# Kernel tuning notes

Measured on AMD Instinct MI355X. Metric: run time of the kernel, lower is better.

The kernel has to match this reference:

```python
import jax, jax.numpy as jnp
import numpy as np

OUT_FEATURES = 4096
IN_FEATURES = 4096
SCALE_EPS = 1e-5


def setup_inputs() -> dict:
    key = jax.random.key(0)
    k1, k2, k3 = jax.random.split(key, 3)
    x = jax.random.normal(k1, (8192, IN_FEATURES), dtype=jnp.float32)
    # packed int4 weights: two signed nibbles per byte-equivalent int
    weight_packed = jax.random.randint(k2, (OUT_FEATURES, IN_FEATURES // 2), 0, 256, dtype=jnp.int32)
    weight_scale = jax.random.uniform(k3, (OUT_FEATURES,), dtype=jnp.float32) * 0.01 + 1e-4
    return {"x": x, "weight_packed": weight_packed, "weight_scale": weight_scale}


def _unpack_int4(weight_packed):
    # low nibble first, then high nibble, sign-extended from 4 bits
    low = weight_packed & 15
    high = (weight_packed >> 4) & 15
    low = jnp.where(low > 7, low - 16, low)
    high = jnp.where(high > 7, high - 16, high)
    # interleave -> [out_features, in_features]
    w_q = jnp.stack([low, high], axis=-1).reshape(weight_packed.shape[0], -1)
    return w_q


def reference(x, weight_packed, weight_scale):
    # per-row activation quantization to int4 range [-8, 7]
    x_max = jnp.max(jnp.abs(x), axis=-1, keepdims=True)
    x_scale = jnp.maximum(x_max / 7.0, SCALE_EPS)          # [tokens, 1]
    x_q = jnp.clip(jnp.round(x / x_scale), -8.0, 7.0)      # float carrier of int4 values

    w_q = _unpack_int4(weight_packed).astype(jnp.float32)  # [out, in]

    out = jnp.einsum('ti,oi->to', x_q, w_q)                # [tokens, out]
    out = out * (x_scale * weight_scale[None, :])
    return out.astype(x.dtype)
```

## Files before the change

### kernel.cpp

```cpp
#include <hip/hip_runtime.h>

#define SCALE_EPS 1e-5f

typedef int v4i __attribute__((ext_vector_type(4)));

static __device__ __forceinline__ void gll16(const void* g, void* l) {
  __builtin_amdgcn_global_load_lds(
      (const __attribute__((address_space(1))) unsigned int*)g,
      (__attribute__((address_space(3))) unsigned int*)l,
      16, 0, 0);
}

__global__ __launch_bounds__(256) void unpack_w(const int* __restrict__ wp,
                                                char* __restrict__ wq) {
  const int kc = blockIdx.x;
  const int nt = blockIdx.y;
  const int tid = threadIdx.x;
  char* tile = wq + ((size_t)nt * 64 + kc) * 8192;
  const int n0 = nt * 128;
#pragma unroll
  for (int j = 0; j < 4; ++j) {
    int u = j * 256 + tid;
    int r = u >> 3;
    int p = u & 7;
    const v4i* src = (const v4i*)((const char*)wp + (size_t)(n0 + r) * 8192 + kc * 128 + p * 16);
    v4i v = *src;
    unsigned int b[8];
#pragma unroll
    for (int q = 0; q < 4; ++q) {
      int lo = ((v[q] & 15) ^ 8) - 8;
      int hi = (((v[q] >> 4) & 15) ^ 8) - 8;
      b[q * 2]     = (unsigned int)(lo & 255);
      b[q * 2 + 1] = (unsigned int)(hi & 255);
    }
    unsigned int w0 = b[0] | (b[1] << 8) | (b[2] << 16) | (b[3] << 24);
    unsigned int w1 = b[4] | (b[5] << 8) | (b[6] << 16) | (b[7] << 24);
    *(uint2*)(tile + (r >> 4) * 1024 + (p >> 1) * 256 + (r & 15) * 16 + (p & 1) * 8) =
        make_uint2(w0, w1);
  }
}

__global__ __launch_bounds__(256) void quant_x(const float* __restrict__ x,
                                               char* __restrict__ xq,
                                               float* __restrict__ xs) {
  __shared__ float lmax[4][4];
  const int tid = threadIdx.x;
  const int w = tid >> 6;
  const int l = tid & 63;
  const int t0 = blockIdx.x * 4;
  const int row = l >> 4;
  const int t = t0 + row;
  const int sub = l & 15;

  const float* base = x + (size_t)t * 4096 + w * 1024 + sub * 4;
  float4 vals[16];
  float m = 0.0f;
#pragma unroll
  for (int s = 0; s < 16; ++s) {
    vals[s] = *(const float4*)(base + s * 64);
    m = fmaxf(m, fmaxf(fmaxf(fabsf(vals[s].x), fabsf(vals[s].y)),
                       fmaxf(fabsf(vals[s].z), fabsf(vals[s].w))));
  }
#pragma unroll
  for (int d = 1; d < 16; d <<= 1) m = fmaxf(m, __shfl_xor(m, d, 64));
  if (sub == 0) lmax[w][row] = m;
  __syncthreads();
  float rm = fmaxf(fmaxf(lmax[0][row], lmax[1][row]),
                   fmaxf(lmax[2][row], lmax[3][row]));
  float scale = fmaxf(rm / 7.0f, SCALE_EPS);
  if (w == 0 && sub == 0) xs[t] = scale;

  const int mt = t0 >> 7;
  const int f = (t0 & 127) >> 4;
  const int r16 = t & 15;
  const int cc = sub >> 2;
  const int b4 = (sub & 3) * 4;

#pragma unroll
  for (int s = 0; s < 16; ++s) {
    float4 v = vals[s];
    int q0 = (int)fminf(fmaxf(rintf(v.x / scale), -8.0f), 7.0f);
    int q1 = (int)fminf(fmaxf(rintf(v.y / scale), -8.0f), 7.0f);
    int q2 = (int)fminf(fmaxf(rintf(v.z / scale), -8.0f), 7.0f);
    int q3 = (int)fminf(fmaxf(rintf(v.w / scale), -8.0f), 7.0f);
    unsigned int wd = (unsigned int)(q0 & 255) | ((unsigned int)(q1 & 255) << 8) |
                      ((unsigned int)(q2 & 255) << 16) | ((unsigned int)(q3 & 255) << 24);
    *(unsigned int*)(xq + ((size_t)mt * 64 + w * 16 + s) * 8192 +
                     f * 1024 + cc * 256 + r16 * 16 + b4) = wd;
  }
}

__global__ __launch_bounds__(512, 2) void gemm_i8(const char* __restrict__ xq,
                                                  const char* __restrict__ wq,
                                                  const float* __restrict__ xs,
                                                  const float* __restrict__ wsc,
                                                  float* __restrict__ out) {
  __shared__ char lds[4][32768];
  const int tid = threadIdx.x;
  const int wid = tid >> 6;
  const int lane = tid & 63;
  const int wm = wid >> 2;
  const int wn = wid & 3;

  const int bid = blockIdx.x;
  const int wg = (bid & 7) * 64 + (bid >> 3);
  const int by = wg >> 4;
  const int bx = wg & 15;

  const char* Asrc0 = xq + (size_t)(2 * by) * 64 * 8192;
  const char* Asrc1 = Asrc0 + 64 * 8192;
  const char* Bsrc0 = wq + (size_t)(2 * bx) * 64 * 8192;
  const char* Bsrc1 = Bsrc0 + 64 * 8192;
  const int toff = tid * 16;

  v4i acc[8][4] = {};

#define STAGE(kt, p)                                                              \
  gll16(((p) == 0 ? Asrc0 : (p) == 1 ? Asrc1 : (p) == 2 ? Bsrc0 : Bsrc1) +        \
            (kt) * 8192 + toff,                                                    \
        lds[(kt) & 3] + (p) * 8192 + toff)

  for (int t = 0; t < 3; ++t) {
    STAGE(t, 0); STAGE(t, 1); STAGE(t, 2); STAGE(t, 3);
  }
  asm volatile("s_waitcnt vmcnt(8)" ::: "memory");
  __builtin_amdgcn_s_barrier();

  auto tile_step = [&](int kt, bool stage, int vm) {
    const char* As = lds[kt & 3];
    const char* Bs = lds[kt & 3] + 16384;
    v4i a[4], b[4];
#pragma unroll
    for (int mi = 0; mi < 4; ++mi)
      a[mi] = *(const v4i*)(As + (wm * 8 + mi) * 1024 + lane * 16);
#pragma unroll
    for (int ni = 0; ni < 4; ++ni)
      b[ni] = *(const v4i*)(Bs + (wn * 4 + ni) * 1024 + lane * 16);
    if (stage) { STAGE(kt + 3, 0); STAGE(kt + 3, 1); }
    __builtin_amdgcn_s_barrier();
    asm volatile("s_waitcnt lgkmcnt(0)" ::: "memory");
    __builtin_amdgcn_sched_barrier(0);
    __builtin_amdgcn_s_setprio(1);
#pragma unroll
    for (int mi = 0; mi < 4; ++mi)
#pragma unroll
      for (int ni = 0; ni < 4; ++ni)
        acc[mi][ni] = __builtin_amdgcn_mfma_i32_16x16x64_i8(a[mi], b[ni], acc[mi][ni], 0, 0, 0);
    __builtin_amdgcn_s_setprio(0);
    __builtin_amdgcn_s_barrier();
#pragma unroll
    for (int mi = 0; mi < 4; ++mi)
      a[mi] = *(const v4i*)(As + (wm * 8 + 4 + mi) * 1024 + lane * 16);
    if (stage) { STAGE(kt + 3, 2); STAGE(kt + 3, 3); }
    if (vm == 8)      asm volatile("s_waitcnt vmcnt(8)" ::: "memory");
    else if (vm == 4) asm volatile("s_waitcnt vmcnt(4)" ::: "memory");
    else if (vm == 0) asm volatile("s_waitcnt vmcnt(0)" ::: "memory");
    __builtin_amdgcn_s_barrier();
    asm volatile("s_waitcnt lgkmcnt(0)" ::: "memory");
    __builtin_amdgcn_sched_barrier(0);
    __builtin_amdgcn_s_setprio(1);
#pragma unroll
    for (int mi = 0; mi < 4; ++mi)
#pragma unroll
      for (int ni = 0; ni < 4; ++ni)
        acc[4 + mi][ni] = __builtin_amdgcn_mfma_i32_16x16x64_i8(a[mi], b[ni], acc[4 + mi][ni], 0, 0, 0);
    __builtin_amdgcn_s_setprio(0);
    __builtin_amdgcn_s_barrier();
  };

  for (int kt = 0; kt < 61; ++kt) tile_step(kt, true, 8);
  tile_step(61, false, 4);
  tile_step(62, false, 0);
  tile_step(63, false, -1);
#undef STAGE

  float wvv[4];
#pragma unroll
  for (int ni = 0; ni < 4; ++ni)
    wvv[ni] = wsc[bx * 256 + wn * 64 + ni * 16 + (lane & 15)];
  const int rbase = by * 256 + wm * 128 + ((lane >> 4) << 2);
  const int cbase = bx * 256 + wn * 64 + (lane & 15);
#pragma unroll
  for (int mi = 0; mi < 8; ++mi) {
#pragma unroll
    for (int j = 0; j < 4; ++j) {
      int t = rbase + mi * 16 + j;
      float xsv = xs[t];
      float* orow = out + (size_t)t * 4096 + cbase;
#pragma unroll
      for (int ni = 0; ni < 4; ++ni)
        orow[ni * 16] = (float)acc[mi][ni][j] * (xsv * wvv[ni]);
    }
  }
}

extern "C" void kernel_launch(void* const* d_in, const int* in_sizes, int n_in,
                              void* d_out, int out_size, void* d_ws, size_t ws_size,
                              hipStream_t stream) {
  const float* x = (const float*)d_in[0];
  const int* wp = (const int*)d_in[1];
  const float* wsc = (const float*)d_in[2];
  float* out = (float*)d_out;
  char* ws = (char*)d_ws;

  char* xq = ws;
  char* wq = ws + 33554432;
  float* xs = (float*)(ws + 33554432 + 16777216);

  hipLaunchKernelGGL(unpack_w, dim3(64, 32), dim3(256), 0, stream, wp, wq);
  hipLaunchKernelGGL(quant_x, dim3(2048), dim3(256), 0, stream, x, xq, xs);
  hipLaunchKernelGGL(gemm_i8, dim3(512), dim3(512), 0, stream, xq, wq, xs, wsc, out);
}
```

Measured before the change: 182.3 us.

## Double-buffer MFMA fragments in registers and cut barriers per k-tile

After: 176.0 us. 3.4% less time.

```diff
diff --git a/kernel.cpp b/kernel.cpp
--- a/kernel.cpp
+++ b/kernel.cpp
@@ -114,65 +114,74 @@
   const int toff = tid * 16;
 
   v4i acc[8][4] = {};
-
-#define STAGE(kt, p)                                                              \
-  gll16(((p) == 0 ? Asrc0 : (p) == 1 ? Asrc1 : (p) == 2 ? Bsrc0 : Bsrc1) +        \
-            (kt) * 8192 + toff,                                                    \
-        lds[(kt) & 3] + (p) * 8192 + toff)
-
-  for (int t = 0; t < 3; ++t) {
-    STAGE(t, 0); STAGE(t, 1); STAGE(t, 2); STAGE(t, 3);
-  }
+  v4i fA[2][8], fB[2][4];
+
+#define STAGE4(kt)                                                      \
+  do {                                                                  \
+    char* dst_ = lds[(kt) & 3] + toff;                                  \
+    gll16(Asrc0 + (size_t)(kt) * 8192 + toff, dst_);                    \
+    gll16(Asrc1 + (size_t)(kt) * 8192 + toff, dst_ + 8192);             \
+    gll16(Bsrc0 + (size_t)(kt) * 8192 + toff, dst_ + 16384);            \
+    gll16(Bsrc1 + (size_t)(kt) * 8192 + toff, dst_ + 24576);            \
+  } while (0)
+
+#define LOADFRAGS(n, kt1)                                               \
+  do {                                                                  \
+    const char* As_ = lds[(kt1) & 3] + wm * 8192 + lane * 16;           \
+    const char* Bs_ = lds[(kt1) & 3] + 16384 + wn * 4096 + lane * 16;   \
+    _Pragma("unroll") for (int mi = 0; mi < 8; ++mi)                    \
+        fA[n][mi] = *(const v4i*)(As_ + mi * 1024);                     \
+    _Pragma("unroll") for (int ni = 0; ni < 4; ++ni)                    \
+        fB[n][ni] = *(const v4i*)(Bs_ + ni * 1024);                     \
+  } while (0)
+
+#define MFMAC(c)                                                        \
+  do {                                                                  \
+    __builtin_amdgcn_s_setprio(1);                                      \
+    _Pragma("unroll") for (int mi = 0; mi < 8; ++mi)                    \
+        _Pragma("unroll") for (int ni = 0; ni < 4; ++ni)                \
+            acc[mi][ni] = __builtin_amdgcn_mfma_i32_16x16x64_i8(        \
+                fA[c][mi], fB[c][ni], acc[mi][ni], 0, 0, 0);            \
+    __builtin_amdgcn_s_setprio(0);                                      \
+  } while (0)
+
+#define ITER(c, n, kt, do_stage, vm)                                    \
+  do {                                                                  \
+    if (do_stage) STAGE4((kt) + 3);                                     \
+    LOADFRAGS(n, (kt) + 1);                                             \
+    __builtin_amdgcn_sched_barrier(0);                                  \
+    MFMAC(c);                                                           \
+    asm volatile("s_waitcnt lgkmcnt(0)" ::: "memory");                  \
+    if ((vm) == 4) asm volatile("s_waitcnt vmcnt(4)" ::: "memory");     \
+    else if ((vm) == 0) asm volatile("s_waitcnt vmcnt(0)" ::: "memory");\
+    __builtin_amdgcn_sched_barrier(0);                                  \
+    __builtin_amdgcn_s_barrier();                                       \
+    __builtin_amdgcn_sched_barrier(0);                                  \
+  } while (0)
+
+  STAGE4(0); STAGE4(1); STAGE4(2);
   asm volatile("s_waitcnt vmcnt(8)" ::: "memory");
   __builtin_amdgcn_s_barrier();
-
-  auto tile_step = [&](int kt, bool stage, int vm) {
-    const char* As = lds[kt & 3];
-    const char* Bs = lds[kt & 3] + 16384;
-    v4i a[4], b[4];
-#pragma unroll
-    for (int mi = 0; mi < 4; ++mi)
-      a[mi] = *(const v4i*)(As + (wm * 8 + mi) * 1024 + lane * 16);
-#pragma unroll
-    for (int ni = 0; ni < 4; ++ni)
-      b[ni] = *(const v4i*)(Bs + (wn * 4 + ni) * 1024 + lane * 16);
-    if (stage) { STAGE(kt + 3, 0); STAGE(kt + 3, 1); }
-    __builtin_amdgcn_s_barrier();
-    asm volatile("s_waitcnt lgkmcnt(0)" ::: "memory");
-    __builtin_amdgcn_sched_barrier(0);
-    __builtin_amdgcn_s_setprio(1);
-#pragma unroll
-    for (int mi = 0; mi < 4; ++mi)
-#pragma unroll
-      for (int ni = 0; ni < 4; ++ni)
-        acc[mi][ni] = __builtin_amdgcn_mfma_i32_16x16x64_i8(a[mi], b[ni], acc[mi][ni], 0, 0, 0);
-    __builtin_amdgcn_s_setprio(0);
-    __builtin_amdgcn_s_barrier();
-#pragma unroll
-    for (int mi = 0; mi < 4; ++mi)
-      a[mi] = *(const v4i*)(As + (wm * 8 + 4 + mi) * 1024 + lane * 16);
-    if (stage) { STAGE(kt + 3, 2); STAGE(kt + 3, 3); }
-    if (vm == 8)      asm volatile("s_waitcnt vmcnt(8)" ::: "memory");
-    else if (vm == 4) asm volatile("s_waitcnt vmcnt(4)" ::: "memory");
-    else if (vm == 0) asm volatile("s_waitcnt vmcnt(0)" ::: "memory");
-    __builtin_amdgcn_s_barrier();
-    asm volatile("s_waitcnt lgkmcnt(0)" ::: "memory");
-    __builtin_amdgcn_sched_barrier(0);
-    __builtin_amdgcn_s_setprio(1);
-#pragma unroll
-    for (int mi = 0; mi < 4; ++mi)
-#pragma unroll
-      for (int ni = 0; ni < 4; ++ni)
-        acc[4 + mi][ni] = __builtin_amdgcn_mfma_i32_16x16x64_i8(a[mi], b[ni], acc[4 + mi][ni], 0, 0, 0);
-    __builtin_amdgcn_s_setprio(0);
-    __builtin_amdgcn_s_barrier();
-  };
-
-  for (int kt = 0; kt < 61; ++kt) tile_step(kt, true, 8);
-  tile_step(61, false, 4);
-  tile_step(62, false, 0);
-  tile_step(63, false, -1);
-#undef STAGE
+  __builtin_amdgcn_sched_barrier(0);
+  LOADFRAGS(0, 0);
+  asm volatile("s_waitcnt vmcnt(4) lgkmcnt(0)" ::: "memory");
+  __builtin_amdgcn_sched_barrier(0);
+  __builtin_amdgcn_s_barrier();
+  __builtin_amdgcn_sched_barrier(0);
+
+  for (int kt = 0; kt < 60; kt += 2) {
+    ITER(0, 1, kt, true, 4);
+    ITER(1, 0, kt + 1, true, 4);
+  }
+  ITER(0, 1, 60, true, 4);
+  ITER(1, 0, 61, false, 0);
+  ITER(0, 1, 62, false, -1);
+  MFMAC(1);
+
+#undef ITER
+#undef MFMAC
+#undef LOADFRAGS
+#undef STAGE4
 
   float wvv[4];
 #pragma unroll
```
